# Performance work log

Measured on AMD Instinct MI355X. Metric: run time of the kernel, lower is better.

Reference implementation:

```python
import jax, jax.numpy as jnp
import numpy as np

NEG = -1e9

def setup_inputs() -> dict:
    key = jax.random.key(0)
    k1, k2, k3 = jax.random.split(key, 3)
    b, t, d = 16, 2048, 64
    q = jax.random.normal(k1, (b, t, d), dtype=jnp.float32)
    k = jax.random.normal(k2, (b, t, d), dtype=jnp.float32)
    v = jax.random.normal(k3, (b, t, d), dtype=jnp.float32)
    return {"q": q, "k": k, "v": v}

def reference(q, k, v):
    # q:[b,tq,d], k:[b,tk,d], v:[b,tk,dv]
    dim_k = k.shape[-1]
    t_q, t_k = q.shape[1], k.shape[1]
    qk = jnp.einsum('bqd,bkd->bqk', q, k) / jnp.sqrt(jnp.float32(dim_k))
    # causal mask: positions j > i are masked (triu with diag offset 1)
    causal = jnp.triu(jnp.ones((t_q, t_k), dtype=bool), k=1)  # [tq,tk]
    qk = jnp.where(causal[None, :, :], NEG, qk)
    sm_qk = jax.nn.softmax(qk, axis=-1)
    out = jnp.einsum('bqk,bkd->bqd', sm_qk, v)
    return (out, sm_qk)
```

## Files before the change

### kernel.cpp

```cpp
#include <hip/hip_runtime.h>
#include <hip/hip_bf16.h>


#define BATCHES 16
#define SEQ 2048
#define DIM 64
#define QB 64
#define KT 64
#define KT1 128
#define NQB (SEQ / QB)
#define KLD 72
#define VLD 72
#define PFLD 68
#define NEL ((size_t)BATCHES * SEQ * DIM)

#define BAR() do { asm volatile("s_waitcnt lgkmcnt(0)" ::: "memory"); \
                   __builtin_amdgcn_s_barrier(); } while (0)

typedef __attribute__((ext_vector_type(8))) short bf16x8;
typedef __attribute__((ext_vector_type(4))) short short4v;
typedef __attribute__((ext_vector_type(4))) float f32x4;

static __device__ __forceinline__ short f2bf(float f) {
    return __builtin_bit_cast(short, __float2bfloat16(f));
}
static __device__ __forceinline__ float bf2f(short s) {
    unsigned int u = ((unsigned int)(unsigned short)s) << 16;
    return __builtin_bit_cast(float, u);
}
static __device__ __forceinline__ void split8(f32x4 a, f32x4 b, float sc,
                                              bf16x8& hh, bf16x8& ll) {
#pragma unroll
    for (int e = 0; e < 4; ++e) {
        float x = a[e] * sc; short hb = f2bf(x);
        hh[e] = hb; ll[e] = f2bf(x - bf2f(hb));
    }
#pragma unroll
    for (int e = 0; e < 4; ++e) {
        float x = b[e] * sc; short hb = f2bf(x);
        hh[4 + e] = hb; ll[4 + e] = f2bf(x - bf2f(hb));
    }
}

__global__ __launch_bounds__(256) void cvt_kv(
    const float* __restrict__ Kg, const float* __restrict__ Vg,
    short* __restrict__ KVh)
{
    const size_t idx = ((size_t)blockIdx.x * 256 + threadIdx.x) * 8;
    const float* src = (idx < NEL) ? (Kg + idx) : (Vg + (idx - NEL));
    f32x4 a = *(const f32x4*)src;
    f32x4 b = *(const f32x4*)(src + 4);
    bf16x8 r;
#pragma unroll
    for (int e = 0; e < 4; ++e) { r[e] = f2bf(a[e]); r[4 + e] = f2bf(b[e]); }
    *(bf16x8*)&KVh[idx] = r;
}

#define SMEM_BYTES 81408

__global__ __launch_bounds__(512, 2) void sdpa_fused(
    const float* __restrict__ Qg, const short* __restrict__ Khg,
    const short* __restrict__ Vhg, float* __restrict__ Og, float* __restrict__ Pg)
{
    const int i = blockIdx.x;
    const int g = i & 7;
    const int j = i >> 3;
    const int b = 2 * g + (j >> 5);
    const int jj = j & 31;
    const int qb = (j < 32) ? jj : (31 - jj);
    const int q0 = qb * QB;

    const int tid = threadIdx.x;
    const int lane = tid & 63;
    const int wave = tid >> 6;
    const int wr = wave & 3;
    const int h  = wave >> 2;
    const int lo = lane & 15;
    const int hi = lane >> 4;
    const bool kStager = (wave < 4);
    const int stid = kStager ? tid : (tid - 256);
    const int sr = stid >> 4;
    const int sc_ = (stid & 15) * 4;
    const int vr = (stid >> 4) * 4;
    const int s1r = tid >> 4;
    const int s1c = (tid & 15) * 4;

    __shared__ __align__(16) char smem[SMEM_BYTES];
    short (*Khi)[KT * KLD]  = reinterpret_cast<short (*)[KT * KLD]>(smem);
    short (*Vt)[DIM * VLD]  = reinterpret_cast<short (*)[DIM * VLD]>(smem + 18432);
    float (*Pf)[QB * PFLD]  = reinterpret_cast<float (*)[QB * PFLD]>(smem + 46080);
    float (*lS)[QB]         = reinterpret_cast<float (*)[QB]>(smem + 80896);
    short (*K1)[KT1 * KLD]  = reinterpret_cast<short (*)[KT1 * KLD]>(smem);

    const float* qB = Qg + (size_t)b * SEQ * DIM;
    const short* kB = Khg + (size_t)b * SEQ * DIM;
    const short* vB = Vhg + (size_t)b * SEQ * DIM;

    bf16x8 qa0h, qa0l, qa1h, qa1l;
    {
        const float* qr = &qB[(size_t)(q0 + wr * 16 + lo) * DIM + hi * 8];
        split8(*(const f32x4*)qr,        *(const f32x4*)(qr + 4),  0.125f, qa0h, qa0l);
        split8(*(const f32x4*)(qr + 32), *(const f32x4*)(qr + 36), 0.125f, qa1h, qa1l);
    }

    const int nkt = qb + 1;

    const int r16z = tid >> 4;
    const int c4z = (tid & 15) * 4;
    float* zrow0 = &Pg[((size_t)(b * SEQ) + (NQB - 1 - qb) * QB + r16z) * SEQ + c4z];
    float* zrow1 = zrow0 + (size_t)32 * SEQ;

    float rl[4] = {0.f, 0.f, 0.f, 0.f};
    {
        const int nkt1 = (nkt + 1) >> 1;
        auto loadK1 = [&](short4v* kp, int t) {
#pragma unroll
            for (int ii = 0; ii < 4; ++ii)
                kp[ii] = *(const short4v*)&kB[(size_t)(t * KT1 + s1r + 32 * ii) * DIM + s1c];
        };
        auto stageK1 = [&](int buf, const short4v* kp) {
#pragma unroll
            for (int ii = 0; ii < 4; ++ii)
                *(short4v*)&K1[buf][(s1r + 32 * ii) * KLD + s1c] = kp[ii];
        };
        short4v kp[4];
        loadK1(kp, 0);
        stageK1(0, kp);
        if (nkt1 > 1) loadK1(kp, 1);
        BAR();
        const int bandMax = q0 + wr * 16 + 15;
        for (int t = 0; t < nkt1; ++t) {
            const int cur = t & 1;
            if (t + 1 < nkt1) {
                stageK1(cur ^ 1, kp);
                if (t + 2 < nkt1) loadK1(kp, t + 2);
            }
            const int base = t * KT1;
#pragma unroll
            for (int nn = 0; nn < 4; ++nn) {
                const int n = 4 * h + nn;
                const int cbase = base + 16 * n;
                if (cbase > bandMax) continue;
                bf16x8 kh0 = *(const bf16x8*)&K1[cur][(16 * n + lo) * KLD + hi * 8];
                bf16x8 kh1 = *(const bf16x8*)&K1[cur][(16 * n + lo) * KLD + 32 + hi * 8];
                f32x4 acc = {0.f, 0.f, 0.f, 0.f};
                __builtin_amdgcn_s_setprio(1);
                acc = __builtin_amdgcn_mfma_f32_16x16x32_bf16(qa0h, kh0, acc, 0, 0, 0);
                acc = __builtin_amdgcn_mfma_f32_16x16x32_bf16(qa1h, kh1, acc, 0, 0, 0);
                __builtin_amdgcn_s_setprio(0);
                if (cbase + 15 <= q0 + wr * 16) {
#pragma unroll
                    for (int jx = 0; jx < 4; ++jx) rl[jx] += __expf(acc[jx]);
                } else {
                    const int col = cbase + lo;
#pragma unroll
                    for (int jx = 0; jx < 4; ++jx)
                        if (col <= q0 + wr * 16 + hi * 4 + jx) rl[jx] += __expf(acc[jx]);
                }
            }
            BAR();
        }
    }
#pragma unroll
    for (int m = 1; m <= 8; m <<= 1)
#pragma unroll
        for (int jx = 0; jx < 4; ++jx) rl[jx] += __shfl_xor(rl[jx], m, 16);
    if (lo == 0) {
#pragma unroll
        for (int jx = 0; jx < 4; ++jx)
            lS[h][wr * 16 + hi * 4 + jx] = rl[jx];
    }
    BAR();
    float il[4];
#pragma unroll
    for (int jx = 0; jx < 4; ++jx) {
        const int row = wr * 16 + hi * 4 + jx;
        il[jx] = 1.0f / (lS[0][row] + lS[1][row]);
    }
    BAR();

    const int n0 = 2 * h;
    f32x4 o2[2];
#pragma unroll
    for (int nn = 0; nn < 2; ++nn) { o2[nn][0] = 0.f; o2[nn][1] = 0.f; o2[nn][2] = 0.f; o2[nn][3] = 0.f; }

    auto loadK = [&](short4v* kp, int kt) {
#pragma unroll
        for (int ii = 0; ii < 4; ++ii)
            kp[ii] = *(const short4v*)&kB[(size_t)(kt * KT + sr + 16 * ii) * DIM + sc_];
    };
    auto loadV = [&](short4v* vp, int kt) {
#pragma unroll
        for (int ii = 0; ii < 4; ++ii)
            vp[ii] = *(const short4v*)&vB[(size_t)(kt * KT + vr + ii) * DIM + sc_];
    };
    auto stageKhi = [&](int buf, const short4v* kp) {
#pragma unroll
        for (int ii = 0; ii < 4; ++ii)
            *(short4v*)&Khi[buf][(sr + 16 * ii) * KLD + sc_] = kp[ii];
    };
    auto stageVt = [&](int buf, const short4v* vp) {
#pragma unroll
        for (int e = 0; e < 4; ++e) {
            short4v tv;
#pragma unroll
            for (int ii = 0; ii < 4; ++ii) tv[ii] = vp[ii][e];
            *(short4v*)&Vt[buf][(sc_ + e) * VLD + vr] = tv;
        }
    };
    auto rowStore = [&](int pbuf, int kt) {
        const int rr = lane >> 4;
        const int cc = (lane & 15) * 4;
        float* dst0 = &Pg[((size_t)(b * SEQ) + q0 + wave * 8 + rr) * SEQ + kt * KT + cc];
        *(f32x4*)dst0 = *(const f32x4*)&Pf[pbuf][(wave * 8 + rr) * PFLD + cc];
        *(f32x4*)(dst0 + (size_t)4 * SEQ) =
            *(const f32x4*)&Pf[pbuf][(wave * 8 + 4 + rr) * PFLD + cc];
    };
    auto pvStep = [&](int pbuf, int vbuf) {
        const float* pr = &Pf[pbuf][(wr * 16 + lo) * PFLD + hi * 8];
        f32x4 a = *(const f32x4*)pr, c2 = *(const f32x4*)(pr + 4);
        f32x4 d = *(const f32x4*)(pr + 32), e2 = *(const f32x4*)(pr + 36);
        bf16x8 pa0, pa1;
#pragma unroll
        for (int e = 0; e < 4; ++e) {
            pa0[e] = f2bf(a[e]); pa0[4 + e] = f2bf(c2[e]);
            pa1[e] = f2bf(d[e]); pa1[4 + e] = f2bf(e2[e]);
        }
        __builtin_amdgcn_s_setprio(1);
#pragma unroll
        for (int nn = 0; nn < 2; ++nn) {
            const int n = n0 + nn;
            bf16x8 vb0 = *(const bf16x8*)&Vt[vbuf][(16 * n + lo) * VLD + hi * 8];
            bf16x8 vb1 = *(const bf16x8*)&Vt[vbuf][(16 * n + lo) * VLD + 32 + hi * 8];
            o2[nn] = __builtin_amdgcn_mfma_f32_16x16x32_bf16(pa0, vb0, o2[nn], 0, 0, 0);
            o2[nn] = __builtin_amdgcn_mfma_f32_16x16x32_bf16(pa1, vb1, o2[nn], 0, 0, 0);
        }
        __builtin_amdgcn_s_setprio(0);
    };

    {
        short4v kp[4], vp[4];
        if (kStager) {
            loadK(kp, 0); stageKhi(0, kp);
            if (nkt > 1) loadK(kp, 1);
        } else {
            loadV(vp, 0); stageVt(0, vp);
            if (nkt > 1) loadV(vp, 1);
        }
        BAR();

        int vstg = 1, vprev = 2;
        for (int kt = 0; kt < nkt; ++kt) {
            const int cur = kt & 1;
            const int pcur = kt & 1;
            if (kt < qb) {
                const int zt = (NQB - qb) + kt;
                const f32x4 zv = {0.f, 0.f, 0.f, 0.f};
                *(f32x4*)&zrow0[zt * KT] = zv;
                *(f32x4*)&zrow1[zt * KT] = zv;
            }
            if (kt + 1 < nkt) {
                if (kStager) {
                    stageKhi(cur ^ 1, kp);
                    if (kt + 2 < nkt) loadK(kp, kt + 2);
                } else {
                    stageVt(vstg, vp);
                    if (kt + 2 < nkt) loadV(vp, kt + 2);
                }
            }
            if (kt > 0) {
                rowStore(pcur ^ 1, kt - 1);
                pvStep(pcur ^ 1, vprev);
            }
#pragma unroll
            for (int nn = 0; nn < 2; ++nn) {
                const int n = n0 + nn;
                const bool fm = (kt == qb) && (n > wr);
                f32x4 acc = {0.f, 0.f, 0.f, 0.f};
                if (!fm) {
                    bf16x8 kh0 = *(const bf16x8*)&Khi[cur][(16 * n + lo) * KLD + hi * 8];
                    bf16x8 kh1 = *(const bf16x8*)&Khi[cur][(16 * n + lo) * KLD + 32 + hi * 8];
                    __builtin_amdgcn_s_setprio(1);
                    acc = __builtin_amdgcn_mfma_f32_16x16x32_bf16(qa0h, kh0, acc, 0, 0, 0);
                    acc = __builtin_amdgcn_mfma_f32_16x16x32_bf16(qa1h, kh1, acc, 0, 0, 0);
                    acc = __builtin_amdgcn_mfma_f32_16x16x32_bf16(qa0l, kh0, acc, 0, 0, 0);
                    acc = __builtin_amdgcn_mfma_f32_16x16x32_bf16(qa1l, kh1, acc, 0, 0, 0);
                    __builtin_amdgcn_s_setprio(0);
                }
                const int col = 16 * n + lo;
#pragma unroll
                for (int jx = 0; jx < 4; ++jx) {
                    const int row = wr * 16 + hi * 4 + jx;
                    const float p = (!fm && (kt < qb || col <= row)) ? __expf(acc[jx]) * il[jx] : 0.f;
                    Pf[pcur][row * PFLD + col] = p;
                }
            }
            BAR();
            vprev = (vprev == 2) ? 0 : vprev + 1;
            vstg  = (vstg  == 2) ? 0 : vstg  + 1;
        }
        {
            const int pl = (nkt - 1) & 1;
            const int vl = (nkt - 1) % 3;
            rowStore(pl, nkt - 1);
            pvStep(pl, vl);
        }
    }

    {
        float* og = &Og[((size_t)(b * SEQ) + q0 + wr * 16 + hi * 4) * DIM + lo];
#pragma unroll
        for (int jx = 0; jx < 4; ++jx)
#pragma unroll
            for (int nn = 0; nn < 2; ++nn)
                og[jx * DIM + (n0 + nn) * 16] = o2[nn][jx];
    }
}

extern "C" void kernel_launch(void* const* d_in, const int* in_sizes, int n_in,
                              void* d_out, int out_size, void* d_ws, size_t ws_size,
                              hipStream_t stream) {
    const float* q = (const float*)d_in[0];
    const float* k = (const float*)d_in[1];
    const float* v = (const float*)d_in[2];
    float* out  = (float*)d_out;
    float* smqk = out + (size_t)BATCHES * SEQ * DIM;
    short* kvh  = (short*)d_ws;

    cvt_kv<<<(int)(2 * NEL / (256 * 8)), 256, 0, stream>>>(k, v, kvh);
    sdpa_fused<<<NQB * BATCHES, 512, 0, stream>>>(q, kvh, kvh + NEL, out, smqk);
}
```

Measured before the change: 79.15 us.

## Load K fragments directly from global into registers, drop K shared staging

Removes the shared-memory K tiles in both the row-sum pass and the main pass. Each wave now loads its own bf16 K MFMA fragments straight from global memory, register double-buffered in the first pass. This frees LDS, cuts its size, and raises launch bounds to 4 blocks per CU for more occupancy, while also removing barriers in the first pass. In exchange K is read from global/L2 redundantly by every wave row group, the first pass loses its 128-wide tile, and register pressure under the tighter launch bound may cause spills.

```diff
diff --git a/kernel.cpp b/kernel.cpp
--- a/kernel.cpp
+++ b/kernel.cpp
@@ -7,9 +7,7 @@
 #define DIM 64
 #define QB 64
 #define KT 64
-#define KT1 128
 #define NQB (SEQ / QB)
-#define KLD 72
 #define VLD 72
 #define PFLD 68
 #define NEL ((size_t)BATCHES * SEQ * DIM)
@@ -56,9 +54,9 @@
     *(bf16x8*)&KVh[idx] = r;
 }
 
-#define SMEM_BYTES 81408
-
-__global__ __launch_bounds__(512, 2) void sdpa_fused(
+#define SMEM_BYTES 62976
+
+__global__ __launch_bounds__(512, 4) void sdpa_fused(
     const float* __restrict__ Qg, const short* __restrict__ Khg,
     const short* __restrict__ Vhg, float* __restrict__ Og, float* __restrict__ Pg)
 {
@@ -75,22 +73,18 @@
     const int wave = tid >> 6;
     const int wr = wave & 3;
     const int h  = wave >> 2;
+    const int n0 = 2 * h;
     const int lo = lane & 15;
     const int hi = lane >> 4;
-    const bool kStager = (wave < 4);
-    const int stid = kStager ? tid : (tid - 256);
-    const int sr = stid >> 4;
+    const bool vStager = (wave >= 4);
+    const int stid = tid & 255;
     const int sc_ = (stid & 15) * 4;
     const int vr = (stid >> 4) * 4;
-    const int s1r = tid >> 4;
-    const int s1c = (tid & 15) * 4;
 
     __shared__ __align__(16) char smem[SMEM_BYTES];
-    short (*Khi)[KT * KLD]  = reinterpret_cast<short (*)[KT * KLD]>(smem);
-    short (*Vt)[DIM * VLD]  = reinterpret_cast<short (*)[DIM * VLD]>(smem + 18432);
-    float (*Pf)[QB * PFLD]  = reinterpret_cast<float (*)[QB * PFLD]>(smem + 46080);
-    float (*lS)[QB]         = reinterpret_cast<float (*)[QB]>(smem + 80896);
-    short (*K1)[KT1 * KLD]  = reinterpret_cast<short (*)[KT1 * KLD]>(smem);
+    short (*Vt)[DIM * VLD]  = reinterpret_cast<short (*)[DIM * VLD]>(smem);
+    float (*Pf)[QB * PFLD]  = reinterpret_cast<float (*)[QB * PFLD]>(smem + 27648);
+    float (*lS)[QB]         = reinterpret_cast<float (*)[QB]>(smem + 62464);
 
     const float* qB = Qg + (size_t)b * SEQ * DIM;
     const short* kB = Khg + (size_t)b * SEQ * DIM;
@@ -104,6 +98,15 @@
     }
 
     const int nkt = qb + 1;
+
+    auto ldK = [&](bf16x8* d, int kt) {
+#pragma unroll
+        for (int nn = 0; nn < 2; ++nn) {
+            const short* base = &kB[(size_t)(kt * KT + 16 * (n0 + nn) + lo) * DIM + hi * 8];
+            d[2 * nn]     = *(const bf16x8*)base;
+            d[2 * nn + 1] = *(const bf16x8*)(base + 32);
+        }
+    };
 
     const int r16z = tid >> 4;
     const int c4z = (tid & 15) * 4;
@@ -112,53 +115,37 @@
 
     float rl[4] = {0.f, 0.f, 0.f, 0.f};
     {
-        const int nkt1 = (nkt + 1) >> 1;
-        auto loadK1 = [&](short4v* kp, int t) {
-#pragma unroll
-            for (int ii = 0; ii < 4; ++ii)
-                kp[ii] = *(const short4v*)&kB[(size_t)(t * KT1 + s1r + 32 * ii) * DIM + s1c];
-        };
-        auto stageK1 = [&](int buf, const short4v* kp) {
-#pragma unroll
-            for (int ii = 0; ii < 4; ++ii)
-                *(short4v*)&K1[buf][(s1r + 32 * ii) * KLD + s1c] = kp[ii];
-        };
-        short4v kp[4];
-        loadK1(kp, 0);
-        stageK1(0, kp);
-        if (nkt1 > 1) loadK1(kp, 1);
-        BAR();
-        const int bandMax = q0 + wr * 16 + 15;
-        for (int t = 0; t < nkt1; ++t) {
-            const int cur = t & 1;
-            if (t + 1 < nkt1) {
-                stageK1(cur ^ 1, kp);
-                if (t + 2 < nkt1) loadK1(kp, t + 2);
-            }
-            const int base = t * KT1;
-#pragma unroll
-            for (int nn = 0; nn < 4; ++nn) {
-                const int n = 4 * h + nn;
-                const int cbase = base + 16 * n;
-                if (cbase > bandMax) continue;
-                bf16x8 kh0 = *(const bf16x8*)&K1[cur][(16 * n + lo) * KLD + hi * 8];
-                bf16x8 kh1 = *(const bf16x8*)&K1[cur][(16 * n + lo) * KLD + 32 + hi * 8];
+        auto tile = [&](const bf16x8* kf, int kt) {
+#pragma unroll
+            for (int nn = 0; nn < 2; ++nn) {
+                const int n = n0 + nn;
+                if (kt == qb && n > wr) continue;
                 f32x4 acc = {0.f, 0.f, 0.f, 0.f};
                 __builtin_amdgcn_s_setprio(1);
-                acc = __builtin_amdgcn_mfma_f32_16x16x32_bf16(qa0h, kh0, acc, 0, 0, 0);
-                acc = __builtin_amdgcn_mfma_f32_16x16x32_bf16(qa1h, kh1, acc, 0, 0, 0);
+                acc = __builtin_amdgcn_mfma_f32_16x16x32_bf16(qa0h, kf[2 * nn], acc, 0, 0, 0);
+                acc = __builtin_amdgcn_mfma_f32_16x16x32_bf16(qa1h, kf[2 * nn + 1], acc, 0, 0, 0);
                 __builtin_amdgcn_s_setprio(0);
-                if (cbase + 15 <= q0 + wr * 16) {
+                if (kt < qb || n < wr) {
 #pragma unroll
                     for (int jx = 0; jx < 4; ++jx) rl[jx] += __expf(acc[jx]);
                 } else {
-                    const int col = cbase + lo;
+                    const int col = 16 * n + lo;
 #pragma unroll
                     for (int jx = 0; jx < 4; ++jx)
-                        if (col <= q0 + wr * 16 + hi * 4 + jx) rl[jx] += __expf(acc[jx]);
+                        if (col <= wr * 16 + hi * 4 + jx) rl[jx] += __expf(acc[jx]);
                 }
             }
-            BAR();
+        };
+        bf16x8 kfa[4], kfb[4];
+        ldK(kfa, 0);
+        int kt = 0;
+        while (true) {
+            if (kt + 1 <= qb) ldK(kfb, kt + 1);
+            tile(kfa, kt);
+            if (++kt > qb) break;
+            if (kt + 1 <= qb) ldK(kfa, kt + 1);
+            tile(kfb, kt);
+            if (++kt > qb) break;
         }
     }
 #pragma unroll
@@ -177,27 +164,15 @@
         const int row = wr * 16 + hi * 4 + jx;
         il[jx] = 1.0f / (lS[0][row] + lS[1][row]);
     }
-    BAR();
-
-    const int n0 = 2 * h;
+
     f32x4 o2[2];
 #pragma unroll
     for (int nn = 0; nn < 2; ++nn) { o2[nn][0] = 0.f; o2[nn][1] = 0.f; o2[nn][2] = 0.f; o2[nn][3] = 0.f; }
 
-    auto loadK = [&](short4v* kp, int kt) {
-#pragma unroll
-        for (int ii = 0; ii < 4; ++ii)
-            kp[ii] = *(const short4v*)&kB[(size_t)(kt * KT + sr + 16 * ii) * DIM + sc_];
-    };
     auto loadV = [&](short4v* vp, int kt) {
 #pragma unroll
         for (int ii = 0; ii < 4; ++ii)
             vp[ii] = *(const short4v*)&vB[(size_t)(kt * KT + vr + ii) * DIM + sc_];
-    };
-    auto stageKhi = [&](int buf, const short4v* kp) {
-#pragma unroll
-        for (int ii = 0; ii < 4; ++ii)
-            *(short4v*)&Khi[buf][(sr + 16 * ii) * KLD + sc_] = kp[ii];
     };
     auto stageVt = [&](int buf, const short4v* vp) {
 #pragma unroll
@@ -239,11 +214,8 @@
     };
 
     {
-        short4v kp[4], vp[4];
-        if (kStager) {
-            loadK(kp, 0); stageKhi(0, kp);
-            if (nkt > 1) loadK(kp, 1);
-        } else {
+        short4v vp[4];
+        if (vStager) {
             loadV(vp, 0); stageVt(0, vp);
             if (nkt > 1) loadV(vp, 1);
         }
@@ -251,22 +223,18 @@
 
         int vstg = 1, vprev = 2;
         for (int kt = 0; kt < nkt; ++kt) {
-            const int cur = kt & 1;
             const int pcur = kt & 1;
+            bf16x8 kf[4];
+            ldK(kf, kt);
             if (kt < qb) {
                 const int zt = (NQB - qb) + kt;
                 const f32x4 zv = {0.f, 0.f, 0.f, 0.f};
                 *(f32x4*)&zrow0[zt * KT] = zv;
                 *(f32x4*)&zrow1[zt * KT] = zv;
             }
-            if (kt + 1 < nkt) {
-                if (kStager) {
-                    stageKhi(cur ^ 1, kp);
-                    if (kt + 2 < nkt) loadK(kp, kt + 2);
-                } else {
-                    stageVt(vstg, vp);
-                    if (kt + 2 < nkt) loadV(vp, kt + 2);
-                }
+            if (kt + 1 < nkt && vStager) {
+                stageVt(vstg, vp);
+                if (kt + 2 < nkt) loadV(vp, kt + 2);
             }
             if (kt > 0) {
                 rowStore(pcur ^ 1, kt - 1);
@@ -278,13 +246,11 @@
                 const bool fm = (kt == qb) && (n > wr);
                 f32x4 acc = {0.f, 0.f, 0.f, 0.f};
                 if (!fm) {
-                    bf16x8 kh0 = *(const bf16x8*)&Khi[cur][(16 * n + lo) * KLD + hi * 8];
-                    bf16x8 kh1 = *(const bf16x8*)&Khi[cur][(16 * n + lo) * KLD + 32 + hi * 8];
                     __builtin_amdgcn_s_setprio(1);
-                    acc = __builtin_amdgcn_mfma_f32_16x16x32_bf16(qa0h, kh0, acc, 0, 0, 0);
-                    acc = __builtin_amdgcn_mfma_f32_16x16x32_bf16(qa1h, kh1, acc, 0, 0, 0);
-                    acc = __builtin_amdgcn_mfma_f32_16x16x32_bf16(qa0l, kh0, acc, 0, 0, 0);
-                    acc = __builtin_amdgcn_mfma_f32_16x16x32_bf16(qa1l, kh1, acc, 0, 0, 0);
+                    acc = __builtin_amdgcn_mfma_f32_16x16x32_bf16(qa0h, kf[2 * nn], acc, 0, 0, 0);
+                    acc = __builtin_amdgcn_mfma_f32_16x16x32_bf16(qa1h, kf[2 * nn + 1], acc, 0, 0, 0);
+                    acc = __builtin_amdgcn_mfma_f32_16x16x32_bf16(qa0l, kf[2 * nn], acc, 0, 0, 0);
+                    acc = __builtin_amdgcn_mfma_f32_16x16x32_bf16(qa1l, kf[2 * nn + 1], acc, 0, 0, 0);
                     __builtin_amdgcn_s_setprio(0);
                 }
                 const int col = 16 * n + lo;
```

Result: slower. 107.1 us (+35.3%).
